# Kernel tuning notes

Measured on AMD Instinct MI355X. Metric: run time of the kernel, lower is better.

The kernel has to match this reference:

```python
import jax, jax.numpy as jnp
import numpy as np

EMBED_DIM = 1024
LAMBDA_INIT = 0.8
EPS = 1e-5


def setup_inputs() -> dict:
    key = jax.random.key(0)
    ks = jax.random.split(key, 8)
    D = EMBED_DIM
    x = jax.random.normal(ks[0], (4, 2048, D), dtype=jnp.float32)
    # torch Linear weight [out, in]; we store transposed [in, out] for x @ W
    s = 1.0 / np.sqrt(D)
    w_q12 = jax.random.uniform(ks[1], (D, 2 * D), jnp.float32, -s, s)
    w_k12 = jax.random.uniform(ks[2], (D, 2 * D), jnp.float32, -s, s)
    w_v = jax.random.uniform(ks[3], (D, D), jnp.float32, -s, s)
    lambda_q1 = 0.1 * jax.random.normal(ks[4], (D,), jnp.float32)
    lambda_k1 = 0.1 * jax.random.normal(ks[5], (D,), jnp.float32)
    lambda_q2 = 0.1 * jax.random.normal(ks[6], (D,), jnp.float32)
    lambda_k2 = 0.1 * jax.random.normal(ks[7], (D,), jnp.float32)
    return {"x": x, "w_q12": w_q12, "w_k12": w_k12, "w_v": w_v,
            "lambda_q1": lambda_q1, "lambda_k1": lambda_k1,
            "lambda_q2": lambda_q2, "lambda_k2": lambda_k2}


def reference(x, w_q12, w_k12, w_v, lambda_q1, lambda_k1, lambda_q2, lambda_k2):
    D = x.shape[-1]
    scale = D ** (-0.25)
    q12 = jnp.einsum('bsd,de->bse', x, w_q12)
    k12 = jnp.einsum('bsd,de->bse', x, w_k12)
    q1, q2 = jnp.split(q12, 2, axis=-1)
    k1, k2 = jnp.split(k12, 2, axis=-1)
    v = jnp.einsum('bsd,de->bse', x, w_v)
    attn1 = jnp.einsum('bqd,bkd->bqk', q1, k1) * scale
    attn2 = jnp.einsum('bqd,bkd->bqk', q2, k2) * scale
    lam1 = jnp.exp(jnp.sum(lambda_q1 * lambda_k1))
    lam2 = jnp.exp(jnp.sum(lambda_q2 * lambda_k2))
    lam_full = lam1 - lam2 + LAMBDA_INIT
    diff = jax.nn.softmax(attn1, axis=-1) - lam_full * jax.nn.softmax(attn2, axis=-1)
    out = jnp.einsum('bqk,bkd->bqd', diff, v)
    # RMSNorm (no affine), then scale by (1 - lambda_init)
    rms = jnp.sqrt(jnp.mean(out * out, axis=-1, keepdims=True) + EPS)
    return (out / rms) * (1.0 - LAMBDA_INIT)
```

## Files before the change

kernel.cpp:

```cpp
#include <hip/hip_runtime.h>

typedef float f32x4 __attribute__((ext_vector_type(4)));
typedef _Float16 h16x8 __attribute__((ext_vector_type(8)));
typedef _Float16 h16x4 __attribute__((ext_vector_type(4)));

#define GLOAD_LDS16(gp, lp) __builtin_amdgcn_global_load_lds(               \
    (const __attribute__((address_space(1))) void*)(gp),                    \
    (__attribute__((address_space(3))) void*)(lp), 16, 0, 0)

__global__ __launch_bounds__(256) void cast_x(const float* __restrict__ x,
                                              _Float16* __restrict__ xh) {
  long i = (long)blockIdx.x * 256 + threadIdx.x;
  f32x4 a = *(const f32x4*)(x + i * 8);
  f32x4 b = *(const f32x4*)(x + i * 8 + 4);
  h16x8 h;
  h[0] = (_Float16)a[0]; h[1] = (_Float16)a[1];
  h[2] = (_Float16)a[2]; h[3] = (_Float16)a[3];
  h[4] = (_Float16)b[0]; h[5] = (_Float16)b[1];
  h[6] = (_Float16)b[2]; h[7] = (_Float16)b[3];
  *(h16x8*)(xh + i * 8) = h;
}

__global__ __launch_bounds__(256) void tcw(const float* __restrict__ in,
                                           _Float16* __restrict__ out,
                                           int Kd, int Nd, float scale) {
  __shared__ float tile[64][65];
  const int t = threadIdx.x;
  const int k0 = blockIdx.y * 64, n0 = blockIdx.x * 64;
  const int tr = t >> 4, tc = (t & 15) * 4;
#pragma unroll
  for (int i = 0; i < 4; ++i) {
    int r = i * 16 + tr;
    f32x4 a = *(const f32x4*)(in + (long)(k0 + r) * Nd + n0 + tc);
    tile[r][tc + 0] = a[0]; tile[r][tc + 1] = a[1];
    tile[r][tc + 2] = a[2]; tile[r][tc + 3] = a[3];
  }
  __syncthreads();
#pragma unroll
  for (int i = 0; i < 4; ++i) {
    int r = i * 16 + tr;
    h16x4 h;
#pragma unroll
    for (int q = 0; q < 4; ++q) h[q] = (_Float16)(tile[tc + q][r] * scale);
    *(h16x4*)(out + (long)(n0 + r) * Kd + k0 + tc) = h;
  }
}

__global__ __launch_bounds__(256) void trans16(const _Float16* __restrict__ in,
                                               _Float16* __restrict__ out,
                                               int R, int Cd, long ibatch, long obatch) {
  __shared__ _Float16 tile[64][72];
  in += (long)blockIdx.z * ibatch;
  out += (long)blockIdx.z * obatch;
  const int t = threadIdx.x;
  const int r0 = blockIdx.y * 64, c0 = blockIdx.x * 64;
  const int tr = t >> 3, tc8 = (t & 7) * 8;
#pragma unroll
  for (int i = 0; i < 2; ++i) {
    int r = i * 32 + tr;
    h16x8 a = *(const h16x8*)(in + (long)(r0 + r) * Cd + c0 + tc8);
    *(h16x8*)(&tile[r][tc8]) = a;
  }
  __syncthreads();
#pragma unroll
  for (int i = 0; i < 2; ++i) {
    int r = i * 32 + tr;
    h16x8 h;
#pragma unroll
    for (int q = 0; q < 8; ++q) h[q] = tile[tc8 + q][r];
    *(h16x8*)(out + (long)(c0 + r) * R + r0 + tc8) = h;
  }
}

__global__ __launch_bounds__(1024) void lambda_k(const float* __restrict__ lq1,
                                                 const float* __restrict__ lk1,
                                                 const float* __restrict__ lq2,
                                                 const float* __restrict__ lk2,
                                                 float* __restrict__ lam) {
  __shared__ float sh1[16], sh2[16];
  const int t = threadIdx.x;
  float p1 = lq1[t] * lk1[t];
  float p2 = lq2[t] * lk2[t];
#pragma unroll
  for (int off = 1; off < 64; off <<= 1) {
    p1 += __shfl_xor(p1, off);
    p2 += __shfl_xor(p2, off);
  }
  if ((t & 63) == 0) { sh1[t >> 6] = p1; sh2[t >> 6] = p2; }
  __syncthreads();
  if (t == 0) {
    float s1 = 0.f, s2 = 0.f;
    for (int i = 0; i < 16; ++i) { s1 += sh1[i]; s2 += sh2[i]; }
    lam[0] = __expf(s1) - __expf(s2) + 0.8f;
  }
}

template <int NREP, typename CT>
__global__ __launch_bounds__(512, 2) void gemmp(
    const _Float16* __restrict__ A, const _Float16* __restrict__ B,
    CT* __restrict__ C, int K, int lda, int ldb, int ldc,
    long abatch, long bbatch, long cbatch, long a2, long c2, int natt,
    int nbx, int nby) {
  constexpr int BN = NREP * 64;
  __shared__ _Float16 As[4][256 * 32];
  __shared__ _Float16 Bs[4][BN * 32];

  const int nwg = gridDim.x;
  const int orig = blockIdx.x;
  const int qd = nwg >> 3, rm = nwg & 7;
  const int xcd = orig & 7, sub = orig >> 3;
  const int wgid = (xcd < rm ? xcd * (qd + 1) : rm * (qd + 1) + (xcd - rm) * qd) + sub;

  const int z = wgid / (nbx * nby);
  const int rem = wgid - z * nbx * nby;
  const int by = rem / nbx;
  const int bx = rem - by * nbx;
  const int att = z % natt;
  const int bz = z / natt;

  const int t = threadIdx.x;
  const int lane = t & 63, wv = t >> 6;
  const int wm = wv >> 2, wn = wv & 3;
  const int lg = lane >> 4, l15 = lane & 15;

  const _Float16* Ab = A + (long)bz * abatch + (long)att * a2 + (long)(by * 256) * lda;
  const _Float16* Bb = B + (long)bz * bbatch + (long)att * a2 + (long)(bx * BN) * ldb;

  const int eA0 = t,       rA0 = eA0 >> 2, sA0 = ((eA0 & 3) - (rA0 >> 1)) & 3;
  const int eA1 = t + 512, rA1 = eA1 >> 2, sA1 = ((eA1 & 3) - (rA1 >> 1)) & 3;
  const long goA0 = (long)rA0 * lda + sA0 * 8;
  const long goA1 = (long)rA1 * lda + sA1 * 8;
  const int eB0 = t,       rB0 = eB0 >> 2, sB0 = ((eB0 & 3) - (rB0 >> 1)) & 3;
  const long goB0 = (long)rB0 * ldb + sB0 * 8;
  const int eB1 = t + 512, rB1 = eB1 >> 2, sB1 = ((eB1 & 3) - (rB1 >> 1)) & 3;
  const long goB1 = (long)rB1 * ldb + sB1 * 8;

  auto stA0 = [&](int S) { GLOAD_LDS16(Ab + goA0 + S * 32, &As[S & 3][eA0 * 8]); };
  auto stA1 = [&](int S) { GLOAD_LDS16(Ab + goA1 + S * 32, &As[S & 3][eA1 * 8]); };
  auto stB0 = [&](int S) { GLOAD_LDS16(Bb + goB0 + S * 32, &Bs[S & 3][eB0 * 8]); };
  auto stB1 = [&](int S) { GLOAD_LDS16(Bb + goB1 + S * 32, &Bs[S & 3][eB1 * 8]); };

  int offA[8], offB[NREP];
#pragma unroll
  for (int m = 0; m < 8; ++m) {
    int r = wm * 128 + m * 16 + l15;
    offA[m] = (r * 4 + ((lg + (r >> 1)) & 3)) * 8;
  }
#pragma unroll
  for (int n = 0; n < NREP; ++n) {
    int r = wn * (NREP * 16) + n * 16 + l15;
    offB[n] = (r * 4 + ((lg + (r >> 1)) & 3)) * 8;
  }

  f32x4 acc[8][NREP] = {};
  const int NS = K >> 5;

  for (int P = 0; P < 3; ++P) {
    stA0(P); stA1(P); stB0(P);
    if constexpr (NREP == 4) stB1(P);
  }
  if constexpr (NREP == 4) asm volatile("s_waitcnt vmcnt(8)" ::: "memory");
  else                     asm volatile("s_waitcnt vmcnt(6)" ::: "memory");
  __builtin_amdgcn_s_barrier();

  for (int S = 0; S < NS; ++S) {
    const int rg = S & 3;
    const _Float16* Asb = &As[rg][0];
    const _Float16* Bsb = &Bs[rg][0];
    const bool pf = (S + 3 < NS);
    h16x8 af[4], bf[NREP];

#pragma unroll
    for (int m = 0; m < 4; ++m) af[m] = *(const h16x8*)(Asb + offA[m]);
#pragma unroll
    for (int n = 0; n < NREP; ++n) bf[n] = *(const h16x8*)(Bsb + offB[n]);
    if (pf) { stA0(S + 3); stA1(S + 3); }
    __builtin_amdgcn_s_barrier();
    __builtin_amdgcn_s_setprio(1);
#pragma unroll
    for (int m = 0; m < 4; ++m)
#pragma unroll
      for (int n = 0; n < NREP; ++n)
        acc[m][n] = __builtin_amdgcn_mfma_f32_16x16x32_f16(af[m], bf[n], acc[m][n], 0, 0, 0);
    __builtin_amdgcn_s_setprio(0);
    __builtin_amdgcn_s_barrier();

#pragma unroll
    for (int m = 0; m < 4; ++m) af[m] = *(const h16x8*)(Asb + offA[4 + m]);
    if (pf) {
      stB0(S + 3);
      if constexpr (NREP == 4) stB1(S + 3);
    }
    {
      const int newer = NS - S - 2;
      if constexpr (NREP == 4) {
        if (newer >= 2)      asm volatile("s_waitcnt vmcnt(8)" ::: "memory");
        else if (newer == 1) asm volatile("s_waitcnt vmcnt(4)" ::: "memory");
        else                 asm volatile("s_waitcnt vmcnt(0)" ::: "memory");
      } else {
        if (newer >= 2)      asm volatile("s_waitcnt vmcnt(6)" ::: "memory");
        else if (newer == 1) asm volatile("s_waitcnt vmcnt(3)" ::: "memory");
        else                 asm volatile("s_waitcnt vmcnt(0)" ::: "memory");
      }
    }
    __builtin_amdgcn_s_barrier();
    __builtin_amdgcn_s_setprio(1);
#pragma unroll
    for (int m = 0; m < 4; ++m)
#pragma unroll
      for (int n = 0; n < NREP; ++n)
        acc[4 + m][n] = __builtin_amdgcn_mfma_f32_16x16x32_f16(af[m], bf[n], acc[4 + m][n], 0, 0, 0);
    __builtin_amdgcn_s_setprio(0);
    __builtin_amdgcn_s_barrier();
  }

  CT* Cb = C + (long)bz * cbatch + (long)att * c2;
  const int crow0 = by * 256 + wm * 128;
  const int ccol0 = bx * BN + wn * (NREP * 16);
#pragma unroll
  for (int m = 0; m < 8; ++m)
#pragma unroll
    for (int n = 0; n < NREP; ++n)
#pragma unroll
      for (int j = 0; j < 4; ++j)
        Cb[(long)(crow0 + m * 16 + lg * 4 + j) * ldc + ccol0 + n * 16 + l15] =
            (CT)acc[m][n][j];
}

__global__ __launch_bounds__(256) void softmax_diff(const _Float16* __restrict__ S1,
                                                    const _Float16* __restrict__ S2,
                                                    _Float16* __restrict__ D,
                                                    const float* __restrict__ lamp) {
  const long row = (long)blockIdx.x * 4 + (threadIdx.x >> 6);
  const int lane = threadIdx.x & 63;
  const float lam = *lamp;
  const _Float16* s1 = S1 + row * 2048;
  const _Float16* s2 = S2 + row * 2048;
  float v1[32], v2[32];
  float m1 = -3e38f, m2 = -3e38f;
#pragma unroll
  for (int j = 0; j < 4; ++j) {
    h16x8 a = ((const h16x8*)s1)[j * 64 + lane];
    h16x8 b = ((const h16x8*)s2)[j * 64 + lane];
#pragma unroll
    for (int q = 0; q < 8; ++q) {
      v1[j * 8 + q] = (float)a[q]; v2[j * 8 + q] = (float)b[q];
      m1 = fmaxf(m1, v1[j * 8 + q]); m2 = fmaxf(m2, v2[j * 8 + q]);
    }
  }
#pragma unroll
  for (int off = 1; off < 64; off <<= 1) {
    m1 = fmaxf(m1, __shfl_xor(m1, off));
    m2 = fmaxf(m2, __shfl_xor(m2, off));
  }
  float l1 = 0.f, l2 = 0.f;
#pragma unroll
  for (int e = 0; e < 32; ++e) {
    v1[e] = __expf(v1[e] - m1); l1 += v1[e];
    v2[e] = __expf(v2[e] - m2); l2 += v2[e];
  }
#pragma unroll
  for (int off = 1; off < 64; off <<= 1) {
    l1 += __shfl_xor(l1, off);
    l2 += __shfl_xor(l2, off);
  }
  const float r1 = 1.f / l1, r2 = lam / l2;
  _Float16* d = D + row * 2048;
#pragma unroll
  for (int j = 0; j < 4; ++j) {
    h16x8 h;
#pragma unroll
    for (int q = 0; q < 8; ++q)
      h[q] = (_Float16)(v1[j * 8 + q] * r1 - v2[j * 8 + q] * r2);
    ((h16x8*)d)[j * 64 + lane] = h;
  }
}

__global__ __launch_bounds__(256) void rmsnorm(const _Float16* __restrict__ O,
                                               float* __restrict__ out) {
  const long row = (long)blockIdx.x * 4 + (threadIdx.x >> 6);
  const int lane = threadIdx.x & 63;
  const _Float16* o = O + row * 1024;
  h16x8 a = ((const h16x8*)o)[lane];
  h16x8 b = ((const h16x8*)o)[64 + lane];
  float xa[8], xb[8];
  float ss = 0.f;
#pragma unroll
  for (int q = 0; q < 8; ++q) {
    xa[q] = (float)a[q]; xb[q] = (float)b[q];
    ss += xa[q] * xa[q] + xb[q] * xb[q];
  }
#pragma unroll
  for (int off = 1; off < 64; off <<= 1) ss += __shfl_xor(ss, off);
  const float s = 0.2f * rsqrtf(ss * (1.f / 1024.f) + 1e-5f);
  float* po = out + row * 1024;
  f32x4 r;
#pragma unroll
  for (int q = 0; q < 4; ++q) r[q] = xa[q] * s;
  *(f32x4*)(po + lane * 8) = r;
#pragma unroll
  for (int q = 0; q < 4; ++q) r[q] = xa[4 + q] * s;
  *(f32x4*)(po + lane * 8 + 4) = r;
#pragma unroll
  for (int q = 0; q < 4; ++q) r[q] = xb[q] * s;
  *(f32x4*)(po + 512 + lane * 8) = r;
#pragma unroll
  for (int q = 0; q < 4; ++q) r[q] = xb[4 + q] * s;
  *(f32x4*)(po + 512 + lane * 8 + 4) = r;
}

extern "C" void kernel_launch(void* const* d_in, const int* in_sizes, int n_in,
                              void* d_out, int out_size, void* d_ws, size_t ws_size,
                              hipStream_t stream) {
  const float* x   = (const float*)d_in[0];
  const float* wq  = (const float*)d_in[1];
  const float* wk  = (const float*)d_in[2];
  const float* wv  = (const float*)d_in[3];
  const float* lq1 = (const float*)d_in[4];
  const float* lk1 = (const float*)d_in[5];
  const float* lq2 = (const float*)d_in[6];
  const float* lk2 = (const float*)d_in[7];
  float* out = (float*)d_out;

  const size_t MB = 1ull << 20;
  char* ws = (char*)d_ws;
  _Float16* xh   = (_Float16*)(ws + 0);
  _Float16* Wp   = (_Float16*)(ws + 16 * MB);
  _Float16* qkv  = (_Float16*)(ws + 26 * MB);
  _Float16* vt   = (_Float16*)(ws + 106 * MB);
  _Float16* S1   = (_Float16*)(ws + 122 * MB);
  _Float16* S2   = (_Float16*)(ws + 154 * MB);
  float*    lam  = (float*)(ws + 186 * MB);
  _Float16* diff = (_Float16*)(ws + 26 * MB);
  _Float16* opre = (_Float16*)(ws + 58 * MB);

  const float scale = 0.17677669529663689f;

  cast_x<<<4096, 256, 0, stream>>>(x, xh);
  tcw<<<dim3(32, 16), 256, 0, stream>>>(wq, Wp, 1024, 2048, scale);
  tcw<<<dim3(32, 16), 256, 0, stream>>>(wk, Wp + 2048l * 1024, 1024, 2048, 1.0f);
  tcw<<<dim3(16, 16), 256, 0, stream>>>(wv, Wp + 4096l * 1024, 1024, 1024, 1.0f);
  lambda_k<<<1, 1024, 0, stream>>>(lq1, lk1, lq2, lk2, lam);

  gemmp<4, _Float16><<<640, 512, 0, stream>>>(xh, Wp, qkv, 1024, 1024, 1024, 5120,
                                              0, 0, 0, 0, 0, 1, 20, 32);

  trans16<<<dim3(16, 32, 4), 256, 0, stream>>>(qkv + 4096, vt, 2048, 5120,
                                               2048l * 5120, 1024l * 2048);

  gemmp<4, _Float16><<<512, 512, 0, stream>>>(qkv, qkv + 2048, S1, 1024, 5120, 5120, 2048,
                                              2048l * 5120, 2048l * 5120, 2048l * 2048,
                                              1024, 16777216l, 2, 8, 8);

  softmax_diff<<<2048, 256, 0, stream>>>(S1, S2, diff, lam);

  gemmp<2, _Float16><<<256, 512, 0, stream>>>(diff, vt, opre, 2048, 2048, 2048, 1024,
                                              2048l * 2048, 1024l * 2048, 2048l * 1024,
                                              0, 0, 1, 8, 8);

  rmsnorm<<<2048, 256, 0, stream>>>(opre, out);
}
```

Baseline: 292.6 us.

## Replace GEMM mainloop with K=64 double-buffered 8-phase ping-pong schedule

Rewrites the shared fp16 MFMA GEMM used by the projection, score and output stages. Each stage now loads a K=64 slice into two LDS buffers with an XOR swizzle and splits the MMA work into eight quadrant phases. LDS fragment reads, global-to-LDS prefetches and fine-grained vmcnt waits are interleaved so that loads overlap the MFMA bursts, and there are fewer barriers per unit of K. The cost is a more intricate hand-counted wait schedule, which risks races or miscounts, plus more fragment registers in flight.

```diff
diff --git a/kernel.cpp b/kernel.cpp
--- a/kernel.cpp
+++ b/kernel.cpp
@@ -7,6 +7,9 @@
 #define GLOAD_LDS16(gp, lp) __builtin_amdgcn_global_load_lds(               \
     (const __attribute__((address_space(1))) void*)(gp),                    \
     (__attribute__((address_space(3))) void*)(lp), 16, 0, 0)
+
+#define BARX do { __builtin_amdgcn_s_barrier(); asm volatile("" ::: "memory"); } while (0)
+#define VMW(N) asm volatile("s_waitcnt vmcnt(" #N ")" ::: "memory")
 
 __global__ __launch_bounds__(256) void cast_x(const float* __restrict__ x,
                                               _Float16* __restrict__ xh) {
@@ -96,20 +99,23 @@
 }
 
 template <int NREP, typename CT>
-__global__ __launch_bounds__(512, 2) void gemmp(
+__global__ __launch_bounds__(512, 2) void gemm8p(
     const _Float16* __restrict__ A, const _Float16* __restrict__ B,
     CT* __restrict__ C, int K, int lda, int ldb, int ldc,
     long abatch, long bbatch, long cbatch, long a2, long c2, int natt,
     int nbx, int nby) {
   constexpr int BN = NREP * 64;
-  __shared__ _Float16 As[4][256 * 32];
-  __shared__ _Float16 Bs[4][BN * 32];
+  constexpr int BHALF = BN / 2;
+  constexpr int BHB = BHALF * 64 * 2;
+  constexpr int NH = NREP / 2;
+  __shared__ _Float16 As[2][2][128][64];
+  __shared__ _Float16 Bs[2][2][BHALF][64];
 
   const int nwg = gridDim.x;
   const int orig = blockIdx.x;
   const int qd = nwg >> 3, rm = nwg & 7;
-  const int xcd = orig & 7, sub = orig >> 3;
-  const int wgid = (xcd < rm ? xcd * (qd + 1) : rm * (qd + 1) + (xcd - rm) * qd) + sub;
+  const int xcd = orig & 7, sub_ = orig >> 3;
+  const int wgid = (xcd < rm ? xcd * (qd + 1) : rm * (qd + 1) + (xcd - rm) * qd) + sub_;
 
   const int z = wgid / (nbx * nby);
   const int rem = wgid - z * nbx * nby;
@@ -126,93 +132,131 @@
   const _Float16* Ab = A + (long)bz * abatch + (long)att * a2 + (long)(by * 256) * lda;
   const _Float16* Bb = B + (long)bz * bbatch + (long)att * a2 + (long)(bx * BN) * ldb;
 
-  const int eA0 = t,       rA0 = eA0 >> 2, sA0 = ((eA0 & 3) - (rA0 >> 1)) & 3;
-  const int eA1 = t + 512, rA1 = eA1 >> 2, sA1 = ((eA1 & 3) - (rA1 >> 1)) & 3;
-  const long goA0 = (long)rA0 * lda + sA0 * 8;
-  const long goA1 = (long)rA1 * lda + sA1 * 8;
-  const int eB0 = t,       rB0 = eB0 >> 2, sB0 = ((eB0 & 3) - (rB0 >> 1)) & 3;
-  const long goB0 = (long)rB0 * ldb + sB0 * 8;
-  const int eB1 = t + 512, rB1 = eB1 >> 2, sB1 = ((eB1 & 3) - (rB1 >> 1)) & 3;
-  const long goB1 = (long)rB1 * ldb + sB1 * 8;
-
-  auto stA0 = [&](int S) { GLOAD_LDS16(Ab + goA0 + S * 32, &As[S & 3][eA0 * 8]); };
-  auto stA1 = [&](int S) { GLOAD_LDS16(Ab + goA1 + S * 32, &As[S & 3][eA1 * 8]); };
-  auto stB0 = [&](int S) { GLOAD_LDS16(Bb + goB0 + S * 32, &Bs[S & 3][eB0 * 8]); };
-  auto stB1 = [&](int S) { GLOAD_LDS16(Bb + goB1 + S * 32, &Bs[S & 3][eB1 * 8]); };
-
-  int offA[8], offB[NREP];
-#pragma unroll
-  for (int m = 0; m < 8; ++m) {
-    int r = wm * 128 + m * 16 + l15;
-    offA[m] = (r * 4 + ((lg + (r >> 1)) & 3)) * 8;
-  }
-#pragma unroll
-  for (int n = 0; n < NREP; ++n) {
-    int r = wn * (NREP * 16) + n * 16 + l15;
-    offB[n] = (r * 4 + ((lg + (r >> 1)) & 3)) * 8;
-  }
-
+  const int rS = t >> 3;
+  const int gsS = (t & 7) ^ (rS & 7);
+  char* AsBase = (char*)&As[0][0][0][0];
+  char* BsBase = (char*)&Bs[0][0][0][0];
+
+  auto stgA = [&](int T) {
+  };
+  auto stgA0 = [&](int T) {
+    const long ko = (long)T * 64 + gsS * 8;
+    char* dst = AsBase + (T & 1) * 32768 + t * 16;
+    GLOAD_LDS16(Ab + (long)rS * lda + ko, dst);
+    GLOAD_LDS16(Ab + (long)(128 + rS) * lda + ko, dst + 16384);
+  };
+  auto stgA1 = [&](int T) {
+    const long ko = (long)T * 64 + gsS * 8;
+    char* dst = AsBase + (T & 1) * 32768 + 8192 + t * 16;
+    GLOAD_LDS16(Ab + (long)(64 + rS) * lda + ko, dst);
+    GLOAD_LDS16(Ab + (long)(192 + rS) * lda + ko, dst + 16384);
+  };
+  auto stgB = [&](int T, int h) {
+    const long ko = (long)T * 64 + gsS * 8;
+    char* dst = BsBase + (T & 1) * (2 * BHB) + h * BHB + t * 16;
+    if constexpr (NREP == 4) {
+      GLOAD_LDS16(Bb + (long)(h * 128 + rS) * ldb + ko, dst);
+      GLOAD_LDS16(Bb + (long)(h * 128 + 64 + rS) * ldb + ko, dst + 8192);
+    } else {
+      GLOAD_LDS16(Bb + (long)(h * 64 + rS) * ldb + ko, dst);
+    }
+  };
+
+  const int b2 = (l15 >> 2) & 1;
+  const int lowsw = (lg ^ (l15 & 3)) * 16 + l15 * 128;
+  const char* pA0 = AsBase + wm * 16384 + lowsw + b2 * 64;
+  const char* pA1 = AsBase + wm * 16384 + lowsw + (1 - b2) * 64;
+  const char* pB0 = BsBase + (wn >> 1) * BHB + (wn & 1) * (BHALF / 2 * 128) + lowsw + b2 * 64;
+  const char* pB1 = pB0 - b2 * 64 + (1 - b2) * 64;
+
+  h16x8 a[4][2], bA[NH][2], bB[NH][2], bC[NH][2];
   f32x4 acc[8][NREP] = {};
-  const int NS = K >> 5;
-
-  for (int P = 0; P < 3; ++P) {
-    stA0(P); stA1(P); stB0(P);
-    if constexpr (NREP == 4) stB1(P);
-  }
-  if constexpr (NREP == 4) asm volatile("s_waitcnt vmcnt(8)" ::: "memory");
-  else                     asm volatile("s_waitcnt vmcnt(6)" ::: "memory");
-  __builtin_amdgcn_s_barrier();
-
-  for (int S = 0; S < NS; ++S) {
-    const int rg = S & 3;
-    const _Float16* Asb = &As[rg][0];
-    const _Float16* Bsb = &Bs[rg][0];
-    const bool pf = (S + 3 < NS);
-    h16x8 af[4], bf[NREP];
-
-#pragma unroll
-    for (int m = 0; m < 4; ++m) af[m] = *(const h16x8*)(Asb + offA[m]);
-#pragma unroll
-    for (int n = 0; n < NREP; ++n) bf[n] = *(const h16x8*)(Bsb + offB[n]);
-    if (pf) { stA0(S + 3); stA1(S + 3); }
-    __builtin_amdgcn_s_barrier();
-    __builtin_amdgcn_s_setprio(1);
-#pragma unroll
-    for (int m = 0; m < 4; ++m)
-#pragma unroll
-      for (int n = 0; n < NREP; ++n)
-        acc[m][n] = __builtin_amdgcn_mfma_f32_16x16x32_f16(af[m], bf[n], acc[m][n], 0, 0, 0);
-    __builtin_amdgcn_s_setprio(0);
-    __builtin_amdgcn_s_barrier();
-
-#pragma unroll
-    for (int m = 0; m < 4; ++m) af[m] = *(const h16x8*)(Asb + offA[4 + m]);
-    if (pf) {
-      stB0(S + 3);
-      if constexpr (NREP == 4) stB1(S + 3);
+
+  auto rdA = [&](int d, int sub) {
+#pragma unroll
+    for (int j = 0; j < 4; ++j) {
+      a[j][0] = *(const h16x8*)(pA0 + d * 32768 + (sub * 4 + j) * 2048);
+      a[j][1] = *(const h16x8*)(pA1 + d * 32768 + (sub * 4 + j) * 2048);
     }
-    {
-      const int newer = NS - S - 2;
-      if constexpr (NREP == 4) {
-        if (newer >= 2)      asm volatile("s_waitcnt vmcnt(8)" ::: "memory");
-        else if (newer == 1) asm volatile("s_waitcnt vmcnt(4)" ::: "memory");
-        else                 asm volatile("s_waitcnt vmcnt(0)" ::: "memory");
-      } else {
-        if (newer >= 2)      asm volatile("s_waitcnt vmcnt(6)" ::: "memory");
-        else if (newer == 1) asm volatile("s_waitcnt vmcnt(3)" ::: "memory");
-        else                 asm volatile("s_waitcnt vmcnt(0)" ::: "memory");
+  };
+  auto rdB = [&](int d, int sub, h16x8 (&dst)[NH][2]) {
+#pragma unroll
+    for (int j = 0; j < NH; ++j) {
+      dst[j][0] = *(const h16x8*)(pB0 + d * (2 * BHB) + (sub * NH + j) * 2048);
+      dst[j][1] = *(const h16x8*)(pB1 + d * (2 * BHB) + (sub * NH + j) * 2048);
+    }
+  };
+  auto QUAD = [&](int ms, int ns, h16x8 (&bS)[NH][2]) {
+#pragma unroll
+    for (int j = 0; j < 4; ++j)
+#pragma unroll
+      for (int n = 0; n < NH; ++n) {
+        const int mi = ms * 4 + j, ni = ns * NH + n;
+        acc[mi][ni] = __builtin_amdgcn_mfma_f32_16x16x32_f16(a[j][0], bS[n][0], acc[mi][ni], 0, 0, 0);
+        acc[mi][ni] = __builtin_amdgcn_mfma_f32_16x16x32_f16(a[j][1], bS[n][1], acc[mi][ni], 0, 0, 0);
       }
-    }
-    __builtin_amdgcn_s_barrier();
-    __builtin_amdgcn_s_setprio(1);
-#pragma unroll
-    for (int m = 0; m < 4; ++m)
-#pragma unroll
-      for (int n = 0; n < NREP; ++n)
-        acc[4 + m][n] = __builtin_amdgcn_mfma_f32_16x16x32_f16(af[m], bf[n], acc[4 + m][n], 0, 0, 0);
-    __builtin_amdgcn_s_setprio(0);
-    __builtin_amdgcn_s_barrier();
-  }
+  };
+#define PQ(MS, NS, BS) do { __builtin_amdgcn_s_setprio(1); QUAD(MS, NS, BS); \
+                            __builtin_amdgcn_s_setprio(0); } while (0)
+
+  const int NT = K >> 6;
+
+  stgB(0, 0); stgA0(0); stgB(0, 1); stgA1(0); stgB(1, 0); stgA0(1);
+  if constexpr (NREP == 4) VMW(6); else VMW(5);
+  BARX;
+  rdB(0, 0, bA);
+
+  for (int T = 0; T < NT - 2; T += 2) {
+    rdA(0, 0); stgB(T + 1, 1);
+    if constexpr (NREP == 4) VMW(8); else VMW(6);
+    BARX; PQ(0, 0, bA); BARX;
+    rdB(0, 1, bB); stgA1(T + 1);
+    if constexpr (NREP == 4) VMW(8); else VMW(6);
+    BARX; PQ(0, 1, bB); BARX;
+    rdA(0, 1); stgB(T + 2, 0);
+    if constexpr (NREP == 4) VMW(4); else VMW(3);
+    BARX; PQ(1, 1, bB); BARX;
+    rdB(1, 0, bC); stgA0(T + 2);
+    if constexpr (NREP == 4) VMW(8); else VMW(6);
+    BARX; PQ(1, 0, bA); BARX;
+    rdA(1, 0); stgB(T + 2, 1);
+    if constexpr (NREP == 4) VMW(8); else VMW(6);
+    BARX; PQ(0, 0, bC); BARX;
+    rdB(1, 1, bB); stgA1(T + 2);
+    if constexpr (NREP == 4) VMW(8); else VMW(6);
+    BARX; PQ(0, 1, bB); BARX;
+    rdA(1, 1); stgB(T + 3, 0);
+    if constexpr (NREP == 4) VMW(4); else VMW(3);
+    BARX; PQ(1, 1, bB); BARX;
+    rdB(0, 0, bA); stgA0(T + 3);
+    if constexpr (NREP == 4) VMW(8); else VMW(6);
+    BARX; PQ(1, 0, bC); BARX;
+  }
+
+  {
+    rdA(0, 0); stgB(NT - 1, 1);
+    if constexpr (NREP == 4) VMW(8); else VMW(6);
+    BARX; PQ(0, 0, bA); BARX;
+    rdB(0, 1, bB); stgA1(NT - 1);
+    if constexpr (NREP == 4) VMW(8); else VMW(6);
+    BARX; PQ(0, 1, bB); BARX;
+    rdA(0, 1);
+    VMW(2);
+    BARX; PQ(1, 1, bB); BARX;
+    rdB(1, 0, bC);
+    if constexpr (NREP == 4) VMW(4); else VMW(3);
+    BARX; PQ(1, 0, bA); BARX;
+    rdA(1, 0);
+    VMW(2);
+    BARX; PQ(0, 0, bC); BARX;
+    rdB(1, 1, bB);
+    VMW(0);
+    BARX; PQ(0, 1, bB); BARX;
+    rdA(1, 1);
+    BARX; PQ(1, 1, bB); BARX;
+    PQ(1, 0, bC);
+  }
+#undef PQ
 
   CT* Cb = C + (long)bz * cbatch + (long)att * c2;
   const int crow0 = by * 256 + wm * 128;
@@ -342,21 +386,21 @@
   tcw<<<dim3(16, 16), 256, 0, stream>>>(wv, Wp + 4096l * 1024, 1024, 1024, 1.0f);
   lambda_k<<<1, 1024, 0, stream>>>(lq1, lk1, lq2, lk2, lam);
 
-  gemmp<4, _Float16><<<640, 512, 0, stream>>>(xh, Wp, qkv, 1024, 1024, 1024, 5120,
-                                              0, 0, 0, 0, 0, 1, 20, 32);
+  gemm8p<4, _Float16><<<640, 512, 0, stream>>>(xh, Wp, qkv, 1024, 1024, 1024, 5120,
+                                               0, 0, 0, 0, 0, 1, 20, 32);
 
   trans16<<<dim3(16, 32, 4), 256, 0, stream>>>(qkv + 4096, vt, 2048, 5120,
                                                2048l * 5120, 1024l * 2048);
 
-  gemmp<4, _Float16><<<512, 512, 0, stream>>>(qkv, qkv + 2048, S1, 1024, 5120, 5120, 2048,
-                                              2048l * 5120, 2048l * 5120, 2048l * 2048,
-                                              1024, 16777216l, 2, 8, 8);
+  gemm8p<4, _Float16><<<512, 512, 0, stream>>>(qkv, qkv + 2048, S1, 1024, 5120, 5120, 2048,
+                                               2048l * 5120, 2048l * 5120, 2048l * 2048,
+                                               1024, 16777216l, 2, 8, 8);
 
   softmax_diff<<<2048, 256, 0, stream>>>(S1, S2, diff, lam);
 
-  gemmp<2, _Float16><<<256, 512, 0, stream>>>(diff, vt, opre, 2048, 2048, 2048, 1024,
-                                              2048l * 2048, 1024l * 2048, 2048l * 1024,
-                                              0, 0, 1, 8, 8);
+  gemm8p<2, _Float16><<<256, 512, 0, stream>>>(diff, vt, opre, 2048, 2048, 2048, 1024,
+                                               2048l * 2048, 1024l * 2048, 2048l * 1024,
+                                               0, 0, 1, 8, 8);
 
   rmsnorm<<<2048, 256, 0, stream>>>(opre, out);
 }
```

Measured after the change: 281.4 us. 3.8% less time.

## Replace GEMM kernel with smaller-tile, triple-buffered, higher-occupancy variant

Applied to the files above, without the earlier changes.

Swaps the 256xBN, 4-stage, two-phase-per-step GEMM for a templated kernel with 256x128 or 128x128 tiles. Each warp holds a 64x64 accumulator, LDS is triple-buffered with a single barrier per K-step, and launch bounds allow 4 blocks per CU. The aim is more blocks in flight, less LDS and register use per block, and fewer barriers per K-step, so memory latency hides better. In exchange, each tile reuses operands less, the grids get larger, and the wait-count logic is simpler and may stall more often.

```diff
diff --git a/kernel.cpp b/kernel.cpp
--- a/kernel.cpp
+++ b/kernel.cpp
@@ -7,6 +7,9 @@
 #define GLOAD_LDS16(gp, lp) __builtin_amdgcn_global_load_lds(               \
     (const __attribute__((address_space(1))) void*)(gp),                    \
     (__attribute__((address_space(3))) void*)(lp), 16, 0, 0)
+
+#define BARX do { __builtin_amdgcn_s_barrier(); asm volatile("" ::: "memory"); } while (0)
+#define VMW(N) asm volatile("s_waitcnt vmcnt(" #N ")" ::: "memory")
 
 __global__ __launch_bounds__(256) void cast_x(const float* __restrict__ x,
                                               _Float16* __restrict__ xh) {
@@ -95,15 +98,19 @@
   }
 }
 
-template <int NREP, typename CT>
-__global__ __launch_bounds__(512, 2) void gemmp(
+template <int MW, int NW, typename CT>
+__global__ __launch_bounds__(MW * NW * 64, 4) void gemmw(
     const _Float16* __restrict__ A, const _Float16* __restrict__ B,
     CT* __restrict__ C, int K, int lda, int ldb, int ldc,
     long abatch, long bbatch, long cbatch, long a2, long c2, int natt,
     int nbx, int nby) {
-  constexpr int BN = NREP * 64;
-  __shared__ _Float16 As[4][256 * 32];
-  __shared__ _Float16 Bs[4][BN * 32];
+  constexpr int BM = MW * 64, BN = NW * 64;
+  constexpr int THREADS = MW * NW * 64;
+  constexpr int nA = BM * 4 / THREADS;
+  constexpr int nB = BN * 4 / THREADS;
+  constexpr int L = nA + nB;
+  __shared__ _Float16 As[3][BM][32];
+  __shared__ _Float16 Bs[3][BN][32];
 
   const int nwg = gridDim.x;
   const int orig = blockIdx.x;
@@ -120,107 +127,81 @@
 
   const int t = threadIdx.x;
   const int lane = t & 63, wv = t >> 6;
-  const int wm = wv >> 2, wn = wv & 3;
+  const int wm = wv >> 1, wn = wv & 1;
   const int lg = lane >> 4, l15 = lane & 15;
 
-  const _Float16* Ab = A + (long)bz * abatch + (long)att * a2 + (long)(by * 256) * lda;
+  const _Float16* Ab = A + (long)bz * abatch + (long)att * a2 + (long)(by * BM) * lda;
   const _Float16* Bb = B + (long)bz * bbatch + (long)att * a2 + (long)(bx * BN) * ldb;
 
-  const int eA0 = t,       rA0 = eA0 >> 2, sA0 = ((eA0 & 3) - (rA0 >> 1)) & 3;
-  const int eA1 = t + 512, rA1 = eA1 >> 2, sA1 = ((eA1 & 3) - (rA1 >> 1)) & 3;
-  const long goA0 = (long)rA0 * lda + sA0 * 8;
-  const long goA1 = (long)rA1 * lda + sA1 * 8;
-  const int eB0 = t,       rB0 = eB0 >> 2, sB0 = ((eB0 & 3) - (rB0 >> 1)) & 3;
-  const long goB0 = (long)rB0 * ldb + sB0 * 8;
-  const int eB1 = t + 512, rB1 = eB1 >> 2, sB1 = ((eB1 & 3) - (rB1 >> 1)) & 3;
-  const long goB1 = (long)rB1 * ldb + sB1 * 8;
-
-  auto stA0 = [&](int S) { GLOAD_LDS16(Ab + goA0 + S * 32, &As[S & 3][eA0 * 8]); };
-  auto stA1 = [&](int S) { GLOAD_LDS16(Ab + goA1 + S * 32, &As[S & 3][eA1 * 8]); };
-  auto stB0 = [&](int S) { GLOAD_LDS16(Bb + goB0 + S * 32, &Bs[S & 3][eB0 * 8]); };
-  auto stB1 = [&](int S) { GLOAD_LDS16(Bb + goB1 + S * 32, &Bs[S & 3][eB1 * 8]); };
-
-  int offA[8], offB[NREP];
-#pragma unroll
-  for (int m = 0; m < 8; ++m) {
-    int r = wm * 128 + m * 16 + l15;
+  auto stage = [&](int slot, int S) {
+    const long ko = (long)S * 32;
+#pragma unroll
+    for (int j = 0; j < nA; ++j) {
+      const int e = t + j * THREADS;
+      const int r = e >> 2;
+      const int gs = ((e & 3) - (r >> 1)) & 3;
+      GLOAD_LDS16(Ab + (long)r * lda + ko + gs * 8, &As[slot][0][0] + e * 8);
+    }
+#pragma unroll
+    for (int j = 0; j < nB; ++j) {
+      const int e = t + j * THREADS;
+      const int r = e >> 2;
+      const int gs = ((e & 3) - (r >> 1)) & 3;
+      GLOAD_LDS16(Bb + (long)r * ldb + ko + gs * 8, &Bs[slot][0][0] + e * 8);
+    }
+  };
+
+  int offA[4], offB[4];
+#pragma unroll
+  for (int m = 0; m < 4; ++m) {
+    const int r = wm * 64 + m * 16 + l15;
     offA[m] = (r * 4 + ((lg + (r >> 1)) & 3)) * 8;
   }
 #pragma unroll
-  for (int n = 0; n < NREP; ++n) {
-    int r = wn * (NREP * 16) + n * 16 + l15;
+  for (int n = 0; n < 4; ++n) {
+    const int r = wn * 64 + n * 16 + l15;
     offB[n] = (r * 4 + ((lg + (r >> 1)) & 3)) * 8;
   }
 
-  f32x4 acc[8][NREP] = {};
+  f32x4 acc[4][4] = {};
   const int NS = K >> 5;
 
-  for (int P = 0; P < 3; ++P) {
-    stA0(P); stA1(P); stB0(P);
-    if constexpr (NREP == 4) stB1(P);
-  }
-  if constexpr (NREP == 4) asm volatile("s_waitcnt vmcnt(8)" ::: "memory");
-  else                     asm volatile("s_waitcnt vmcnt(6)" ::: "memory");
-  __builtin_amdgcn_s_barrier();
+  stage(0, 0); stage(1, 1);
+  int cur = 0, nx2 = 2;
 
   for (int S = 0; S < NS; ++S) {
-    const int rg = S & 3;
-    const _Float16* Asb = &As[rg][0];
-    const _Float16* Bsb = &Bs[rg][0];
-    const bool pf = (S + 3 < NS);
-    h16x8 af[4], bf[NREP];
-
-#pragma unroll
-    for (int m = 0; m < 4; ++m) af[m] = *(const h16x8*)(Asb + offA[m]);
-#pragma unroll
-    for (int n = 0; n < NREP; ++n) bf[n] = *(const h16x8*)(Bsb + offB[n]);
-    if (pf) { stA0(S + 3); stA1(S + 3); }
-    __builtin_amdgcn_s_barrier();
+    if (S == NS - 1) VMW(0);
+    else { if constexpr (L == 3) VMW(3); else VMW(4); }
+    BARX;
+
+    if (S + 2 < NS) stage(nx2, S + 2);
+
+    const _Float16* Ap = &As[cur][0][0];
+    const _Float16* Bp = &Bs[cur][0][0];
+    h16x8 a[4], b[4];
+#pragma unroll
+    for (int m = 0; m < 4; ++m) a[m] = *(const h16x8*)(Ap + offA[m]);
+#pragma unroll
+    for (int n = 0; n < 4; ++n) b[n] = *(const h16x8*)(Bp + offB[n]);
     __builtin_amdgcn_s_setprio(1);
 #pragma unroll
     for (int m = 0; m < 4; ++m)
 #pragma unroll
-      for (int n = 0; n < NREP; ++n)
-        acc[m][n] = __builtin_amdgcn_mfma_f32_16x16x32_f16(af[m], bf[n], acc[m][n], 0, 0, 0);
+      for (int n = 0; n < 4; ++n)
+        acc[m][n] = __builtin_amdgcn_mfma_f32_16x16x32_f16(a[m], b[n], acc[m][n], 0, 0, 0);
     __builtin_amdgcn_s_setprio(0);
-    __builtin_amdgcn_s_barrier();
-
-#pragma unroll
-    for (int m = 0; m < 4; ++m) af[m] = *(const h16x8*)(Asb + offA[4 + m]);
-    if (pf) {
-      stB0(S + 3);
-      if constexpr (NREP == 4) stB1(S + 3);
-    }
-    {
-      const int newer = NS - S - 2;
-      if constexpr (NREP == 4) {
-        if (newer >= 2)      asm volatile("s_waitcnt vmcnt(8)" ::: "memory");
-        else if (newer == 1) asm volatile("s_waitcnt vmcnt(4)" ::: "memory");
-        else                 asm volatile("s_waitcnt vmcnt(0)" ::: "memory");
-      } else {
-        if (newer >= 2)      asm volatile("s_waitcnt vmcnt(6)" ::: "memory");
-        else if (newer == 1) asm volatile("s_waitcnt vmcnt(3)" ::: "memory");
-        else                 asm volatile("s_waitcnt vmcnt(0)" ::: "memory");
-      }
-    }
-    __builtin_amdgcn_s_barrier();
-    __builtin_amdgcn_s_setprio(1);
-#pragma unroll
-    for (int m = 0; m < 4; ++m)
-#pragma unroll
-      for (int n = 0; n < NREP; ++n)
-        acc[4 + m][n] = __builtin_amdgcn_mfma_f32_16x16x32_f16(af[m], bf[n], acc[4 + m][n], 0, 0, 0);
-    __builtin_amdgcn_s_setprio(0);
-    __builtin_amdgcn_s_barrier();
+
+    cur = (cur == 2) ? 0 : cur + 1;
+    nx2 = (nx2 == 2) ? 0 : nx2 + 1;
   }
 
   CT* Cb = C + (long)bz * cbatch + (long)att * c2;
-  const int crow0 = by * 256 + wm * 128;
-  const int ccol0 = bx * BN + wn * (NREP * 16);
-#pragma unroll
-  for (int m = 0; m < 8; ++m)
-#pragma unroll
-    for (int n = 0; n < NREP; ++n)
+  const int crow0 = by * BM + wm * 64;
+  const int ccol0 = bx * BN + wn * 64;
+#pragma unroll
+  for (int m = 0; m < 4; ++m)
+#pragma unroll
+    for (int n = 0; n < 4; ++n)
 #pragma unroll
       for (int j = 0; j < 4; ++j)
         Cb[(long)(crow0 + m * 16 + lg * 4 + j) * ldc + ccol0 + n * 16 + l15] =
@@ -342,21 +323,21 @@
   tcw<<<dim3(16, 16), 256, 0, stream>>>(wv, Wp + 4096l * 1024, 1024, 1024, 1.0f);
   lambda_k<<<1, 1024, 0, stream>>>(lq1, lk1, lq2, lk2, lam);
 
-  gemmp<4, _Float16><<<640, 512, 0, stream>>>(xh, Wp, qkv, 1024, 1024, 1024, 5120,
-                                              0, 0, 0, 0, 0, 1, 20, 32);
+  gemmw<4, 2, _Float16><<<1280, 512, 0, stream>>>(xh, Wp, qkv, 1024, 1024, 1024, 5120,
+                                                  0, 0, 0, 0, 0, 1, 40, 32);
 
   trans16<<<dim3(16, 32, 4), 256, 0, stream>>>(qkv + 4096, vt, 2048, 5120,
                                                2048l * 5120, 1024l * 2048);
 
-  gemmp<4, _Float16><<<512, 512, 0, stream>>>(qkv, qkv + 2048, S1, 1024, 5120, 5120, 2048,
-                                              2048l * 5120, 2048l * 5120, 2048l * 2048,
-                                              1024, 16777216l, 2, 8, 8);
+  gemmw<4, 2, _Float16><<<1024, 512, 0, stream>>>(qkv, qkv + 2048, S1, 1024, 5120, 5120, 2048,
+                                                  2048l * 5120, 2048l * 5120, 2048l * 2048,
+                                                  1024, 16777216l, 2, 16, 8);
 
   softmax_diff<<<2048, 256, 0, stream>>>(S1, S2, diff, lam);
 
-  gemmp<2, _Float16><<<256, 512, 0, stream>>>(diff, vt, opre, 2048, 2048, 2048, 1024,
-                                              2048l * 2048, 1024l * 2048, 2048l * 1024,
-                                              0, 0, 1, 8, 8);
+  gemmw<2, 2, _Float16><<<512, 256, 0, stream>>>(diff, vt, opre, 2048, 2048, 2048, 1024,
+                                                 2048l * 2048, 1024l * 2048, 2048l * 1024,
+                                                 0, 0, 1, 8, 16);
 
   rmsnorm<<<2048, 256, 0, stream>>>(opre, out);
 }
```

Result: faster. 286.6 us (-2.1%).
